# Kernel optimization log

Hardware: AMD Instinct MI355X
Metric: run time of the kernel (lower is better)

Reference implementation:

```python
import jax, jax.numpy as jnp
import numpy as np

NUM_GRAPHS = 64
NEG_SLOPE_EDGE = 0.2   # GATLayer alpha
NEG_SLOPE_READ = 0.01  # torch default leaky_relu slope in ReadoutLayer


def leaky_relu(x, slope):
    return jnp.where(x >= 0, x, slope * x)


def segment_softmax(e, seg, n):
    # numerically stable softmax of edge logits grouped by destination node
    m = jax.ops.segment_max(e, seg, num_segments=n)
    m = jnp.where(jnp.isfinite(m), m, 0.0)  # guard nodes with no in-edges
    ex = jnp.exp(e - m[seg])
    s = jax.ops.segment_sum(ex, seg, num_segments=n)
    return ex / jnp.where(s > 0, s, 1.0)[seg]


def gat_layer(h, src, dst, e_feat, W, a):
    n = h.shape[0]
    out = W.shape[1]
    z = h @ W                                      # [N, out]
    a_src, a_dst, a_e = a[:out], a[out:2 * out], a[2 * out:]
    # concat([z_src, z_dst, e_feat]) @ a  ==  z_src@a_src + z_dst@a_dst + e@a_e
    logits = leaky_relu(z[src] @ a_src + z[dst] @ a_dst + e_feat @ a_e,
                        NEG_SLOPE_EDGE)            # [E]
    alpha = segment_softmax(logits, dst, n)        # [E]
    msg = alpha[:, None] * z[src]                  # [E, out]
    return jax.ops.segment_sum(msg, dst, num_segments=n)  # [N, out]


def readout(h, gid, w_att, b_att):
    # DGL mean_nodes(g, 'z', 'att'): multiply feat by weight, then mean per graph
    att = jnp.exp(leaky_relu(h @ w_att + b_att, NEG_SLOPE_READ))  # [N]
    num = jax.ops.segment_sum(att[:, None] * h, gid, num_segments=NUM_GRAPHS)
    cnt = jax.ops.segment_sum(jnp.ones_like(att), gid, num_segments=NUM_GRAPHS)
    return num / jnp.maximum(cnt, 1.0)[:, None]    # [G, hidden]


def setup_inputs() -> dict:
    key = jax.random.key(0)
    ks = jax.random.split(key, 16)
    N, E, F_IN, H, ED, C = 50000, 800000, 128, 128, 16, 10
    sc = lambda f: np.float32(1.0 / np.sqrt(f))
    return {
        "x": jax.random.normal(ks[0], (N, F_IN), jnp.float32),
        "e_feat": jax.random.normal(ks[1], (E, ED), jnp.float32),
        "src": jax.random.randint(ks[2], (E,), 0, N, dtype=jnp.int32),
        "dst": jax.random.randint(ks[3], (E,), 0, N, dtype=jnp.int32),
        "gid": jnp.sort(jax.random.randint(ks[4], (N,), 0, NUM_GRAPHS, dtype=jnp.int32)),
        "W1": jax.random.normal(ks[5], (F_IN, H), jnp.float32) * sc(F_IN),
        "a1": jax.random.normal(ks[6], (2 * H + ED,), jnp.float32) * sc(2 * H + ED),
        "W2": jax.random.normal(ks[7], (H, H), jnp.float32) * sc(H),
        "a2": jax.random.normal(ks[8], (2 * H + ED,), jnp.float32) * sc(2 * H + ED),
        "W3": jax.random.normal(ks[9], (H, H), jnp.float32) * sc(H),
        "a3": jax.random.normal(ks[10], (2 * H + ED,), jnp.float32) * sc(2 * H + ED),
        "w_att": jax.random.normal(ks[11], (H,), jnp.float32) * sc(H),
        "b_att": jnp.zeros((), jnp.float32),
        "W_cls": jax.random.normal(ks[12], (3 * H, C), jnp.float32) * sc(3 * H),
        "b_cls": jnp.zeros((C,), jnp.float32),
    }


def reference(x, e_feat, src, dst, gid, W1, a1, W2, a2, W3, a3,
              w_att, b_att, W_cls, b_cls):
    # dropout is identity at inference (training=False)
    h1 = jax.nn.relu(gat_layer(x, src, dst, e_feat, W1, a1))
    hg1 = readout(h1, gid, w_att, b_att)
    h2 = jax.nn.relu(gat_layer(h1, src, dst, e_feat, W2, a2))
    hg2 = readout(h2, gid, w_att, b_att)
    h3 = jax.nn.relu(gat_layer(h2, src, dst, e_feat, W3, a3))
    hg3 = readout(h3, gid, w_att, b_att)
    y = jnp.concatenate([hg1, hg2, hg3], axis=1) @ W_cls + b_cls  # [G, C]
    return jax.nn.log_softmax(y, axis=1)
```

## Files before the change

### kernel.cpp

```cpp
#include <hip/hip_runtime.h>
#include <math.h>

#define HD 128
#define ED 16
#define NG 64
#define NC 10
#define HK 8

typedef short bf16x8 __attribute__((ext_vector_type(8)));
typedef float f32x4 __attribute__((ext_vector_type(4)));

__device__ __forceinline__ unsigned short f2b(float x){
  unsigned u = __float_as_uint(x);
  unsigned r = (u + 0x7fffu + ((u >> 16) & 1u)) >> 16;
  return (unsigned short)r;
}
__device__ __forceinline__ float blo(unsigned p){ return __uint_as_float(p << 16); }
__device__ __forceinline__ float bhi(unsigned p){ return __uint_as_float(p & 0xffff0000u); }
__device__ __forceinline__ float bperm_f(int idx, float v){
  return __int_as_float(__builtin_amdgcn_ds_bpermute(idx<<2, __float_as_int(v)));
}
__device__ __forceinline__ int bperm_i(int idx, int v){
  return __builtin_amdgcn_ds_bpermute(idx<<2, v);
}
__device__ __forceinline__ bf16x8 ld8f32_bf16(const float* p){
  float4 u0 = *(const float4*)p;
  float4 u1 = *(const float4*)(p+4);
  uint4 o;
  o.x = f2b(u0.x) | ((unsigned)f2b(u0.y)<<16);
  o.y = f2b(u0.z) | ((unsigned)f2b(u0.w)<<16);
  o.z = f2b(u1.x) | ((unsigned)f2b(u1.y)<<16);
  o.w = f2b(u1.z) | ((unsigned)f2b(u1.w)<<16);
  return __builtin_bit_cast(bf16x8, o);
}

__global__ __launch_bounds__(256) void k_pre(
    const int* __restrict__ dst, int* __restrict__ h, int Nr,
    int* __restrict__ rank, int E, int NH, int NE4,
    const int* __restrict__ src, const float* __restrict__ ef,
    const float* __restrict__ a1e, const float* __restrict__ a2e,
    const float* __restrict__ a3e, uint2* __restrict__ pay,
    const float* __restrict__ W1, const float* __restrict__ W2, const float* __restrict__ W3,
    unsigned short* __restrict__ Wb,
    const int* __restrict__ gid, float* __restrict__ cnt,
    float* __restrict__ hg,
    int N){
  int b = blockIdx.x;
  if(b < NH){
    int xcc;
    asm volatile("s_getreg_b32 %0, hwreg(HW_REG_XCC_ID, 0, 4)" : "=s"(xcc));
    xcc &= (HK-1);
    int* hk = h + (size_t)xcc*Nr;
    int tag = xcc << 24;
    int e4 = (b*256 + threadIdx.x)*4;
    if(e4+3 < E){
      int4 d = *(const int4*)&dst[e4];
      int4 r;
      r.x = __hip_atomic_fetch_add(&hk[d.x], 1, __ATOMIC_RELAXED, __HIP_MEMORY_SCOPE_WORKGROUP) | tag;
      r.y = __hip_atomic_fetch_add(&hk[d.y], 1, __ATOMIC_RELAXED, __HIP_MEMORY_SCOPE_WORKGROUP) | tag;
      r.z = __hip_atomic_fetch_add(&hk[d.z], 1, __ATOMIC_RELAXED, __HIP_MEMORY_SCOPE_WORKGROUP) | tag;
      r.w = __hip_atomic_fetch_add(&hk[d.w], 1, __ATOMIC_RELAXED, __HIP_MEMORY_SCOPE_WORKGROUP) | tag;
      *(int4*)&rank[e4] = r;
    } else {
      for(int k=0;k<4;k++) if(e4+k<E)
        rank[e4+k] = __hip_atomic_fetch_add(&hk[dst[e4+k]], 1, __ATOMIC_RELAXED, __HIP_MEMORY_SCOPE_WORKGROUP) | tag;
    }
    return;
  }
  b -= NH;
  if(b < NE4){
    int t = b*256 + threadIdx.x;
    int e = t >> 2;
    int sub = t & 3;
    if(e >= E) return;
    float4 f  = *(const float4*)&ef[(size_t)e*ED + sub*4];
    float4 A1 = *(const float4*)&a1e[sub*4];
    float4 A2 = *(const float4*)&a2e[sub*4];
    float4 A3 = *(const float4*)&a3e[sub*4];
    float q1 = fmaf(f.x,A1.x, fmaf(f.y,A1.y, fmaf(f.z,A1.z, f.w*A1.w)));
    float q2 = fmaf(f.x,A2.x, fmaf(f.y,A2.y, fmaf(f.z,A2.z, f.w*A2.w)));
    float q3 = fmaf(f.x,A3.x, fmaf(f.y,A3.y, fmaf(f.z,A3.z, f.w*A3.w)));
    q1 += __shfl_xor(q1,1); q1 += __shfl_xor(q1,2);
    q2 += __shfl_xor(q2,1); q2 += __shfl_xor(q2,2);
    q3 += __shfl_xor(q3,1); q3 += __shfl_xor(q3,2);
    if(sub == 0){
      uint2 A;
      A.x = (unsigned)f2b(q1) | ((unsigned)f2b(q2) << 16);
      A.y = (unsigned)src[e] | ((unsigned)f2b(q3) << 16);
      pay[e] = A;
    }
    return;
  }
  b -= NE4;
  if(b < 24){
    int idx = b*256 + threadIdx.x;
    if(idx >= 3*2048) return;
    int layer = idx >> 11;
    int r = idx & 2047;
    const float* W = (layer==0)?W1:((layer==1)?W2:W3);
    int lane = r & 63, tile = r >> 6;
    int kt = tile >> 3, nt = tile & 7;
    int qq = lane >> 4, cc = lane & 15;
    int kbase = kt*32 + qq*8;
    int col = nt*16 + cc;
    unsigned short tmp[8];
    #pragma unroll
    for(int j=0;j<8;j++) tmp[j] = f2b(W[(size_t)(kbase+j)*HD + col]);
    uint4 o;
    o.x = tmp[0]|((unsigned)tmp[1]<<16); o.y = tmp[2]|((unsigned)tmp[3]<<16);
    o.z = tmp[4]|((unsigned)tmp[5]<<16); o.w = tmp[6]|((unsigned)tmp[7]<<16);
    *(uint4*)&Wb[(size_t)idx*8] = o;
    return;
  }
  b -= 24;
  if(b == 0){
    int g = threadIdx.x;
    if(g >= NG) return;
    int lo=0, hi=N;
    while(lo<hi){ int mid=(lo+hi)>>1; if(gid[mid] < g) lo=mid+1; else hi=mid; }
    int start = lo; lo = start; hi = N;
    while(lo<hi){ int mid=(lo+hi)>>1; if(gid[mid] < g+1) lo=mid+1; else hi=mid; }
    cnt[g] = (float)(lo - start);
    return;
  }
  b -= 1;
  int i = (b*256 + threadIdx.x)*4;
  if(i < 3*NG*HD) *(float4*)&hg[i] = (float4){0.f,0.f,0.f,0.f};
}

__global__ __launch_bounds__(64) void k_bsum(const int* __restrict__ h, int Nr,
                                             int* __restrict__ deg,
                                             int* __restrict__ bsum, int N){
  int b = blockIdx.x, t = threadIdx.x;
  int i = b*256 + t*4;
  int d0=0,d1=0,d2=0,d3=0;
  if(i+3 < N){
    #pragma unroll
    for(int k=0;k<HK;k++){
      int4 v = *(const int4*)&h[(size_t)k*Nr + i];
      d0+=v.x; d1+=v.y; d2+=v.z; d3+=v.w;
    }
    int4 o; o.x=d0; o.y=d1; o.z=d2; o.w=d3;
    *(int4*)&deg[i] = o;
  } else {
    int tmp[4] = {0,0,0,0};
    for(int j=0;j<4;j++) if(i+j<N){
      int s2=0;
      for(int k=0;k<HK;k++) s2 += h[(size_t)k*Nr + i + j];
      deg[i+j]=s2; tmp[j]=s2;
    }
    d0=tmp[0]; d1=tmp[1]; d2=tmp[2]; d3=tmp[3];
  }
  int s = d0+d1+d2+d3;
  #pragma unroll
  for(int o=32;o;o>>=1) s += __shfl_xor(s,o);
  if(t==0) bsum[b] = s;
}

__global__ __launch_bounds__(256) void k_bprop2(const int* __restrict__ deg,
                                                const int* __restrict__ bsum,
                                                const int* __restrict__ h, int Nr,
                                                int* __restrict__ offs,
                                                int* __restrict__ offs2,
                                                int N, int E){
  __shared__ int sh[256];
  __shared__ int sbase;
  int b = blockIdx.x, t = threadIdx.x;
  int s = 0;
  for(int j=t; j<b; j+=256) s += bsum[j];
  #pragma unroll
  for(int o=32;o;o>>=1) s += __shfl_xor(s,o);
  if(t < 4) sh[t] = 0;
  __syncthreads();
  if((t&63)==0) sh[t>>6] = s;
  __syncthreads();
  if(t==0) sbase = sh[0]+sh[1]+sh[2]+sh[3];
  __syncthreads();
  int i = b*256 + t;
  int v = (i<N) ? deg[i] : 0;
  sh[t] = v; __syncthreads();
  for(int o=1;o<256;o<<=1){ int u = (t>=o)?sh[t-o]:0; __syncthreads(); sh[t]+=u; __syncthreads(); }
  if(i<N){
    int base = sbase + sh[t] - v;
    offs[i] = base;
    int run = base;
    #pragma unroll
    for(int k=0;k<HK;k++){
      offs2[(size_t)k*Nr + i] = run;
      run += h[(size_t)k*Nr + i];
    }
  }
  if(b==0 && t==0) offs[N] = E;
}


__device__ __forceinline__ void scatter_dev(int bidx,
                           const int* __restrict__ dst, const int* __restrict__ rank,
                           const uint2* __restrict__ pay,
                           const int* __restrict__ offs2, int Nr,
                           uint2* __restrict__ rec, int E){
  int e = bidx*256 + threadIdx.x;
  if(e >= E) return;
  int d = dst[e];
  unsigned rk = (unsigned)rank[e];
  int k = (int)(rk >> 24);
  int p = offs2[(size_t)k*Nr + d] + (int)(rk & 0xffffffu);
  rec[p] = pay[e];
}

__device__ __forceinline__ void gemm_dev(int bidx,
    const unsigned short* __restrict__ Ab,
    const float* __restrict__ Af,
    const unsigned short* __restrict__ Wb,
    unsigned short* __restrict__ Zb,
    const float* __restrict__ avec,
    float* __restrict__ ps, float* __restrict__ pd, int M)
{
  int tid = threadIdx.x;
  int w = tid >> 6, lane = tid & 63;
  int q = lane >> 4, c = lane & 15;
  int rowbase = bidx*128 + w*32;
  f32x4 acc[2][8];
  #pragma unroll
  for(int t=0;t<2;t++)
    #pragma unroll
    for(int n=0;n<8;n++) acc[t][n] = (f32x4){0.f,0.f,0.f,0.f};

  int r0 = rowbase + c;      if(r0 > M-1) r0 = M-1;
  int r1 = rowbase + 16 + c; if(r1 > M-1) r1 = M-1;
  #pragma unroll
  for(int kt=0; kt<4; kt++){
    int ko = kt*32 + q*8;
    bf16x8 a0, a1;
    if(Af){
      a0 = ld8f32_bf16(&Af[(size_t)r0*HD + ko]);
      a1 = ld8f32_bf16(&Af[(size_t)r1*HD + ko]);
    } else {
      a0 = __builtin_bit_cast(bf16x8, *(const uint4*)&Ab[(size_t)r0*HD + ko]);
      a1 = __builtin_bit_cast(bf16x8, *(const uint4*)&Ab[(size_t)r1*HD + ko]);
    }
    #pragma unroll
    for(int n=0;n<8;n++){
      bf16x8 b = __builtin_bit_cast(bf16x8, *(const uint4*)&Wb[(((size_t)(kt*8+n))*64 + lane)*8]);
      acc[0][n] = __builtin_amdgcn_mfma_f32_16x16x32_bf16(a0, b, acc[0][n], 0,0,0);
      acc[1][n] = __builtin_amdgcn_mfma_f32_16x16x32_bf16(a1, b, acc[1][n], 0,0,0);
    }
  }
  float asv[8], adv[8];
  #pragma unroll
  for(int n=0;n<8;n++){ asv[n] = avec[n*16+c]; adv[n] = avec[HD + n*16+c]; }
  #pragma unroll
  for(int t=0;t<2;t++){
    #pragma unroll
    for(int r=0;r<4;r++){
      int grow = rowbase + t*16 + 4*q + r;
      bool ok = grow < M;
      #pragma unroll
      for(int n=0;n<8;n++){
        if(ok) Zb[(size_t)grow*HD + n*16 + c] = f2b(acc[t][n][r]);
      }
      float pp = 0.f, dd = 0.f;
      #pragma unroll
      for(int n=0;n<8;n++){ pp = fmaf(acc[t][n][r], asv[n], pp); dd = fmaf(acc[t][n][r], adv[n], dd); }
      #pragma unroll
      for(int o=1;o<16;o<<=1){ pp += __shfl_xor(pp,o); dd += __shfl_xor(dd,o); }
      if(ok && c==0){ ps[grow] = pp; pd[grow] = dd; }
    }
  }
}

#define RCH 16
__device__ __forceinline__ void readout_dev(int rb,
                          const unsigned* __restrict__ hbu,
                          const float* __restrict__ att,
                          const int* __restrict__ gid,
                          float* __restrict__ hg, int N){
  int g = rb >> 2;
  int chunk = ((rb & 3) << 2) + (threadIdx.x >> 6);
  int t = threadIdx.x & 63;
  int lo=0, hi=N;
  while(lo<hi){ int mid=(lo+hi)>>1; if(gid[mid] < g) lo=mid+1; else hi=mid; }
  int start = lo; lo = start; hi = N;
  while(lo<hi){ int mid=(lo+hi)>>1; if(gid[mid] < g+1) lo=mid+1; else hi=mid; }
  int end = lo;
  int len = end - start;
  int c0 = start + (int)(((long long)len * chunk) / RCH);
  int c1 = start + (int)(((long long)len * (chunk+1)) / RCH);
  float acc0 = 0.f, acc1 = 0.f;
  for(int v=c0; v<c1; v++){
    unsigned P = hbu[(size_t)v*64 + t];
    float a = att[v];
    acc0 = fmaf(a, blo(P), acc0);
    acc1 = fmaf(a, bhi(P), acc1);
  }
  atomicAdd(&hg[g*HD + 2*t],     acc0);
  atomicAdd(&hg[g*HD + 2*t + 1], acc1);
}

__global__ __launch_bounds__(256) void k_sg1(
    const float* __restrict__ x, const unsigned short* __restrict__ Wb,
    unsigned short* __restrict__ Zb, const float* __restrict__ avec,
    float* __restrict__ ps, float* __restrict__ pd, int M, int GB,
    const int* __restrict__ dst, const int* __restrict__ rank,
    const uint2* __restrict__ pay,
    const int* __restrict__ offs2, int Nr, uint2* __restrict__ rec, int E){
  if(blockIdx.x < GB) gemm_dev(blockIdx.x, (const unsigned short*)0, x, Wb, Zb, avec, ps, pd, M);
  else scatter_dev(blockIdx.x - GB, dst, rank, pay, offs2, Nr, rec, E);
}

__global__ __launch_bounds__(256) void k_rg(
    const unsigned short* __restrict__ Ab, const unsigned short* __restrict__ Wb,
    unsigned short* __restrict__ Zb, const float* __restrict__ avec,
    float* __restrict__ ps, float* __restrict__ pd, int M, int GB,
    const unsigned* __restrict__ hbu, const float* __restrict__ att,
    const int* __restrict__ gid, float* __restrict__ hg, int N){
  if(blockIdx.x < GB) gemm_dev(blockIdx.x, Ab, (const float*)0, Wb, Zb, avec, ps, pd, M);
  else readout_dev(blockIdx.x - GB, hbu, att, gid, hg, N);
}

__global__ __launch_bounds__(256) void k_agg2(const uint4* __restrict__ zb4,
                                              const int* __restrict__ offs,
                                              const uint2* __restrict__ rec,
                                              const float* __restrict__ ps,
                                              const float* __restrict__ pd,
                                              int layer,
                                              unsigned* __restrict__ hbu,
                                              float* __restrict__ att,
                                              const float* __restrict__ watt,
                                              const float* __restrict__ batt, int N){
  int wid = blockIdx.x*4 + (threadIdx.x>>6);
  int lane = threadIdx.x & 63;
  if(wid >= N) return;
  int q = lane >> 4, c = lane & 15;
  int d0 = offs[wid], d1 = offs[wid+1];
  float pdv = pd[wid];
  float acc[8];
  #pragma unroll
  for(int i=0;i<8;i++) acc[i]=0.f;
  float ssum = 0.f;

  for(int t0=d0; t0<d1; t0+=64){
    int rem = d1 - t0; if(rem > 64) rem = 64;
    int j = t0 + lane;
    float w = 0.f; int u = 0;
    if(j < d1){
      uint2 R = rec[j];
      u = (int)(R.y & 0xffffu);
      unsigned qb = (layer==0) ? (R.x & 0xffffu) : (layer==1 ? (R.x >> 16) : (R.y >> 16));
      float ql = __uint_as_float(qb << 16);
      float l = ps[u] + pdv + ql;
      l = (l >= 0.f) ? l : 0.2f*l;
      w = __expf(l);
    }
    float ws = w;
    #pragma unroll
    for(int o=32;o;o>>=1) ws += __shfl_xor(ws,o);
    ssum += ws;
    for(int jb=0; jb<rem; jb+=16){
      float w0 = bperm_f(jb+q,    w);  int u0 = bperm_i(jb+q,    u);
      float w1 = bperm_f(jb+4+q,  w);  int u1 = bperm_i(jb+4+q,  u);
      float w2 = bperm_f(jb+8+q,  w);  int u2 = bperm_i(jb+8+q,  u);
      float w3 = bperm_f(jb+12+q, w);  int u3 = bperm_i(jb+12+q, u);
      uint4 P0 = zb4[(size_t)u0*16 + c];
      uint4 P1 = zb4[(size_t)u1*16 + c];
      uint4 P2 = zb4[(size_t)u2*16 + c];
      uint4 P3 = zb4[(size_t)u3*16 + c];
      acc[0] = fmaf(w0, blo(P0.x), acc[0]); acc[1] = fmaf(w0, bhi(P0.x), acc[1]);
      acc[2] = fmaf(w0, blo(P0.y), acc[2]); acc[3] = fmaf(w0, bhi(P0.y), acc[3]);
      acc[4] = fmaf(w0, blo(P0.z), acc[4]); acc[5] = fmaf(w0, bhi(P0.z), acc[5]);
      acc[6] = fmaf(w0, blo(P0.w), acc[6]); acc[7] = fmaf(w0, bhi(P0.w), acc[7]);
      acc[0] = fmaf(w1, blo(P1.x), acc[0]); acc[1] = fmaf(w1, bhi(P1.x), acc[1]);
      acc[2] = fmaf(w1, blo(P1.y), acc[2]); acc[3] = fmaf(w1, bhi(P1.y), acc[3]);
      acc[4] = fmaf(w1, blo(P1.z), acc[4]); acc[5] = fmaf(w1, bhi(P1.z), acc[5]);
      acc[6] = fmaf(w1, blo(P1.w), acc[6]); acc[7] = fmaf(w1, bhi(P1.w), acc[7]);
      acc[0] = fmaf(w2, blo(P2.x), acc[0]); acc[1] = fmaf(w2, bhi(P2.x), acc[1]);
      acc[2] = fmaf(w2, blo(P2.y), acc[2]); acc[3] = fmaf(w2, bhi(P2.y), acc[3]);
      acc[4] = fmaf(w2, blo(P2.z), acc[4]); acc[5] = fmaf(w2, bhi(P2.z), acc[5]);
      acc[6] = fmaf(w2, blo(P2.w), acc[6]); acc[7] = fmaf(w2, bhi(P2.w), acc[7]);
      acc[0] = fmaf(w3, blo(P3.x), acc[0]); acc[1] = fmaf(w3, bhi(P3.x), acc[1]);
      acc[2] = fmaf(w3, blo(P3.y), acc[2]); acc[3] = fmaf(w3, bhi(P3.y), acc[3]);
      acc[4] = fmaf(w3, blo(P3.z), acc[4]); acc[5] = fmaf(w3, bhi(P3.z), acc[5]);
      acc[6] = fmaf(w3, blo(P3.w), acc[6]); acc[7] = fmaf(w3, bhi(P3.w), acc[7]);
    }
  }
  #pragma unroll
  for(int i=0;i<8;i++){ acc[i] += __shfl_xor(acc[i],16); acc[i] += __shfl_xor(acc[i],32); }
  float inv = (d1 > d0) ? 1.0f/ssum : 0.0f;
  #pragma unroll
  for(int i=0;i<8;i++) acc[i] = fmaxf(acc[i]*inv, 0.f);
  hbu[(size_t)wid*64 + c*4 + q] = (unsigned)f2b(acc[2*q]) | ((unsigned)f2b(acc[2*q+1])<<16);
  float4 w0v = *(const float4*)&watt[c*8];
  float4 w1v = *(const float4*)&watt[c*8+4];
  float t = acc[0]*w0v.x + acc[1]*w0v.y + acc[2]*w0v.z + acc[3]*w0v.w
          + acc[4]*w1v.x + acc[5]*w1v.y + acc[6]*w1v.z + acc[7]*w1v.w;
  #pragma unroll
  for(int o=1;o<16;o<<=1) t += __shfl_xor(t,o);
  t += batt[0];
  float lr = (t >= 0.f) ? t : 0.01f*t;
  if(lane==0) att[wid] = __expf(lr);
}

__global__ __launch_bounds__(64) void k_readout(const unsigned* __restrict__ hbu,
                                                const float* __restrict__ att,
                                                const int* __restrict__ gid,
                                                float* __restrict__ hg, int N){
  int g = blockIdx.x / RCH;
  int chunk = blockIdx.x % RCH;
  int t = threadIdx.x;
  int lo=0, hi=N;
  while(lo<hi){ int mid=(lo+hi)>>1; if(gid[mid] < g) lo=mid+1; else hi=mid; }
  int start = lo; lo = start; hi = N;
  while(lo<hi){ int mid=(lo+hi)>>1; if(gid[mid] < g+1) lo=mid+1; else hi=mid; }
  int end = lo;
  int len = end - start;
  int c0 = start + (int)(((long long)len * chunk) / RCH);
  int c1 = start + (int)(((long long)len * (chunk+1)) / RCH);
  float acc0 = 0.f, acc1 = 0.f;
  for(int v=c0; v<c1; v++){
    unsigned P = hbu[(size_t)v*64 + t];
    float a = att[v];
    acc0 = fmaf(a, blo(P), acc0);
    acc1 = fmaf(a, bhi(P), acc1);
  }
  atomicAdd(&hg[g*HD + 2*t],     acc0);
  atomicAdd(&hg[g*HD + 2*t + 1], acc1);
}

__global__ __launch_bounds__(384) void k_final(const float* __restrict__ hg,
                                               const float* __restrict__ cnt,
                                               const float* __restrict__ Wc,
                                               const float* __restrict__ bc,
                                               float* __restrict__ out){
  int g = blockIdx.x;
  int t = threadIdx.x;
  __shared__ float red[6];
  __shared__ float yv[NC];
  float invc = 1.f / fmaxf(cnt[g], 1.f);
  int part = t >> 7;
  int f = t & 127;
  float v = hg[(size_t)part*NG*HD + g*HD + f] * invc;
  for(int c=0; c<NC; c++){
    float p = v * Wc[(size_t)t*NC + c];
    #pragma unroll
    for(int o=32;o;o>>=1) p += __shfl_xor(p,o);
    if((t&63)==0) red[t>>6] = p;
    __syncthreads();
    if(t==0) yv[c] = bc[c] + red[0]+red[1]+red[2]+red[3]+red[4]+red[5];
    __syncthreads();
  }
  if(t==0){
    float mx = -INFINITY;
    #pragma unroll
    for(int c=0;c<NC;c++) mx = fmaxf(mx, yv[c]);
    float s = 0.f;
    #pragma unroll
    for(int c=0;c<NC;c++) s += __expf(yv[c] - mx);
    float ls = logf(s);
    #pragma unroll
    for(int c=0;c<NC;c++) out[g*NC + c] = yv[c] - mx - ls;
  }
}

extern "C" void kernel_launch(void* const* d_in, const int* in_sizes, int n_in,
                              void* d_out, int out_size, void* d_ws, size_t ws_size,
                              hipStream_t stream) {
  const float* x     = (const float*)d_in[0];
  const float* efeat = (const float*)d_in[1];
  const int*   src   = (const int*)d_in[2];
  const int*   dst   = (const int*)d_in[3];
  const int*   gid   = (const int*)d_in[4];
  const float* W1    = (const float*)d_in[5];
  const float* a1    = (const float*)d_in[6];
  const float* W2    = (const float*)d_in[7];
  const float* a2    = (const float*)d_in[8];
  const float* W3    = (const float*)d_in[9];
  const float* a3    = (const float*)d_in[10];
  const float* watt  = (const float*)d_in[11];
  const float* batt  = (const float*)d_in[12];
  const float* Wc    = (const float*)d_in[13];
  const float* bc    = (const float*)d_in[14];
  float* out = (float*)d_out;

  int N = in_sizes[4];
  int E = in_sizes[2];
  int Nr = (N + 63) & ~63;

  char* p = (char*)d_ws;
  auto alloc = [&](size_t bytes)->void*{
    void* r = (void*)p;
    p += (bytes + 255) & ~(size_t)255;
    return r;
  };
  unsigned short* Hb = (unsigned short*)alloc((size_t)N*HD*2);
  unsigned short* Zb = (unsigned short*)alloc((size_t)N*HD*2);
  unsigned short* Wball = (unsigned short*)alloc((size_t)3*2048*8*2);
  float* ps      = (float*)alloc((size_t)N*4);
  float* pd      = (float*)alloc((size_t)N*4);
  float* att     = (float*)alloc((size_t)N*4);
  int*   deg     = (int*)  alloc((size_t)N*4);
  int*   offs    = (int*)  alloc((size_t)(N+1)*4);
  int*   offs2   = (int*)  alloc((size_t)Nr*HK*4);
  int*   h       = (int*)  alloc((size_t)Nr*HK*4);
  int*   rank    = (int*)  alloc((size_t)E*4);
  uint2* pay     = (uint2*)alloc((size_t)E*8);
  uint2* rec     = (uint2*)alloc((size_t)E*8);
  int*   bsum    = (int*)  alloc((size_t)1024*4);
  float* hg      = (float*)alloc((size_t)3*NG*HD*4);
  float* cnt     = (float*)alloc((size_t)NG*4);
  (void)ws_size; (void)n_in; (void)out_size;

  int nwblocks = (N + 3) / 4;
  int nb = (N + 255) / 256;
  int NH = (E/4 + 255) / 256;
  int NE4 = (E*4 + 255) / 256;
  int GB = (N + 127) / 128;
  int SB = (E + 255) / 256;

  hipMemsetAsync(h, 0, (size_t)Nr*HK*4, stream);
  k_pre<<<NH + NE4 + 24 + 1 + 24, 256, 0, stream>>>(dst, h, Nr, rank, E, NH, NE4,
                                                    src, efeat, a1+2*HD, a2+2*HD, a3+2*HD, pay,
                                                    W1, W2, W3, Wball,
                                                    gid, cnt, hg, N);
  k_bsum<<<nb, 64, 0, stream>>>(h, Nr, deg, bsum, N);
  k_bprop2<<<nb, 256, 0, stream>>>(deg, bsum, h, Nr, offs, offs2, N, E);
  k_sg1<<<GB + SB, 256, 0, stream>>>(x, Wball, Zb, a1, ps, pd, N, GB,
                                     dst, rank, pay, offs2, Nr, rec, E);
  k_agg2<<<nwblocks, 256, 0, stream>>>((const uint4*)Zb, offs, rec, ps, pd, 0,
                                       (unsigned*)Hb, att, watt, batt, N);
  k_rg<<<GB + NG*4, 256, 0, stream>>>(Hb, Wball + (size_t)1*2048*8, Zb, a2, ps, pd, N, GB,
                                      (const unsigned*)Hb, att, gid, hg + 0*NG*HD, N);
  k_agg2<<<nwblocks, 256, 0, stream>>>((const uint4*)Zb, offs, rec, ps, pd, 1,
                                       (unsigned*)Hb, att, watt, batt, N);
  k_rg<<<GB + NG*4, 256, 0, stream>>>(Hb, Wball + (size_t)2*2048*8, Zb, a3, ps, pd, N, GB,
                                      (const unsigned*)Hb, att, gid, hg + 1*NG*HD, N);
  k_agg2<<<nwblocks, 256, 0, stream>>>((const uint4*)Zb, offs, rec, ps, pd, 2,
                                       (unsigned*)Hb, att, watt, batt, N);
  k_readout<<<NG*RCH, 64, 0, stream>>>((const unsigned*)Hb, att, gid,
                                       hg + 2*NG*HD, N);
  k_final<<<NG, 384, 0, stream>>>(hg, cnt, Wc, bc, out);
}
```

Measured before the change: 398.2 us.

## Replace global per-XCC atomic histogram with LDS-chunked per-block histograms

The in-degree count for the CSR build no longer uses global atomics into eight per-XCC histograms. Each block now takes a contiguous chunk of 16K edges and histograms it in shared memory with packed 16-bit counters, making several passes over the node range. It writes per-block 16-bit counts, and the rank is derived from the edge's block index. The degree-sum step is folded into k_pre, which drops the memset and the k_bsum launch. In exchange, each block rereads its dst chunk once per node pass, and the prefix and scatter steps loop over about 49 block histograms instead of 8.

New measurement: 448.6 us. 12.7% more time.

```diff
diff --git a/kernel.cpp b/kernel.cpp
--- a/kernel.cpp
+++ b/kernel.cpp
@@ -5,7 +5,8 @@
 #define ED 16
 #define NG 64
 #define NC 10
-#define HK 8
+#define EPB_LOG 14
+#define EPB (1<<EPB_LOG)
 
 typedef short bf16x8 __attribute__((ext_vector_type(8)));
 typedef float f32x4 __attribute__((ext_vector_type(4)));
@@ -34,9 +35,38 @@
   return __builtin_bit_cast(bf16x8, o);
 }
 
+__global__ __launch_bounds__(256) void k_hist(const int* __restrict__ dst,
+                                              unsigned short* __restrict__ H16, int Nr2,
+                                              int* __restrict__ rank, int E, int N){
+  __shared__ unsigned hls[EPB/2];
+  int kb = blockIdx.x;
+  int e0 = kb << EPB_LOG;
+  int e1 = e0 + EPB; if(e1 > E) e1 = E;
+  int npass = (N + EPB - 1) >> EPB_LOG;
+  for(int ps=0; ps<npass; ps++){
+    int h0 = ps << EPB_LOG;
+    for(int w=threadIdx.x; w<EPB/2; w+=256) hls[w] = 0u;
+    __syncthreads();
+    for(int e=e0+threadIdx.x; e<e1; e+=256){
+      int d = dst[e];
+      unsigned rel = (unsigned)(d - h0);
+      if(rel < (unsigned)EPB){
+        unsigned add = (rel & 1u) ? 0x10000u : 1u;
+        unsigned old = atomicAdd(&hls[rel>>1], add);
+        rank[e] = (int)((old >> ((rel & 1u)*16u)) & 0xffffu);
+      }
+    }
+    __syncthreads();
+    int nodes = N - h0; if(nodes > EPB) nodes = EPB;
+    int words = (nodes + 1) >> 1;
+    unsigned* Hg = (unsigned*)(H16 + (size_t)kb*Nr2 + h0);
+    for(int w=threadIdx.x; w<words; w+=256) Hg[w] = hls[w];
+    __syncthreads();
+  }
+}
+
 __global__ __launch_bounds__(256) void k_pre(
-    const int* __restrict__ dst, int* __restrict__ h, int Nr,
-    int* __restrict__ rank, int E, int NH, int NE4,
+    int NE4, int E,
     const int* __restrict__ src, const float* __restrict__ ef,
     const float* __restrict__ a1e, const float* __restrict__ a2e,
     const float* __restrict__ a3e, uint2* __restrict__ pay,
@@ -44,30 +74,10 @@
     unsigned short* __restrict__ Wb,
     const int* __restrict__ gid, float* __restrict__ cnt,
     float* __restrict__ hg,
+    const unsigned short* __restrict__ H16, int Nr2, int NB,
+    int* __restrict__ deg, int* __restrict__ bsum,
     int N){
   int b = blockIdx.x;
-  if(b < NH){
-    int xcc;
-    asm volatile("s_getreg_b32 %0, hwreg(HW_REG_XCC_ID, 0, 4)" : "=s"(xcc));
-    xcc &= (HK-1);
-    int* hk = h + (size_t)xcc*Nr;
-    int tag = xcc << 24;
-    int e4 = (b*256 + threadIdx.x)*4;
-    if(e4+3 < E){
-      int4 d = *(const int4*)&dst[e4];
-      int4 r;
-      r.x = __hip_atomic_fetch_add(&hk[d.x], 1, __ATOMIC_RELAXED, __HIP_MEMORY_SCOPE_WORKGROUP) | tag;
-      r.y = __hip_atomic_fetch_add(&hk[d.y], 1, __ATOMIC_RELAXED, __HIP_MEMORY_SCOPE_WORKGROUP) | tag;
-      r.z = __hip_atomic_fetch_add(&hk[d.z], 1, __ATOMIC_RELAXED, __HIP_MEMORY_SCOPE_WORKGROUP) | tag;
-      r.w = __hip_atomic_fetch_add(&hk[d.w], 1, __ATOMIC_RELAXED, __HIP_MEMORY_SCOPE_WORKGROUP) | tag;
-      *(int4*)&rank[e4] = r;
-    } else {
-      for(int k=0;k<4;k++) if(e4+k<E)
-        rank[e4+k] = __hip_atomic_fetch_add(&hk[dst[e4+k]], 1, __ATOMIC_RELAXED, __HIP_MEMORY_SCOPE_WORKGROUP) | tag;
-    }
-    return;
-  }
-  b -= NH;
   if(b < NE4){
     int t = b*256 + threadIdx.x;
     int e = t >> 2;
@@ -124,45 +134,34 @@
     return;
   }
   b -= 1;
-  int i = (b*256 + threadIdx.x)*4;
-  if(i < 3*NG*HD) *(float4*)&hg[i] = (float4){0.f,0.f,0.f,0.f};
-}
-
-__global__ __launch_bounds__(64) void k_bsum(const int* __restrict__ h, int Nr,
-                                             int* __restrict__ deg,
-                                             int* __restrict__ bsum, int N){
-  int b = blockIdx.x, t = threadIdx.x;
-  int i = b*256 + t*4;
-  int d0=0,d1=0,d2=0,d3=0;
-  if(i+3 < N){
-    #pragma unroll
-    for(int k=0;k<HK;k++){
-      int4 v = *(const int4*)&h[(size_t)k*Nr + i];
-      d0+=v.x; d1+=v.y; d2+=v.z; d3+=v.w;
-    }
-    int4 o; o.x=d0; o.y=d1; o.z=d2; o.w=d3;
-    *(int4*)&deg[i] = o;
-  } else {
-    int tmp[4] = {0,0,0,0};
-    for(int j=0;j<4;j++) if(i+j<N){
-      int s2=0;
-      for(int k=0;k<HK;k++) s2 += h[(size_t)k*Nr + i + j];
-      deg[i+j]=s2; tmp[j]=s2;
-    }
-    d0=tmp[0]; d1=tmp[1]; d2=tmp[2]; d3=tmp[3];
-  }
-  int s = d0+d1+d2+d3;
-  #pragma unroll
-  for(int o=32;o;o>>=1) s += __shfl_xor(s,o);
-  if(t==0) bsum[b] = s;
+  if(b < 24){
+    int i = (b*256 + threadIdx.x)*4;
+    if(i < 3*NG*HD) *(float4*)&hg[i] = (float4){0.f,0.f,0.f,0.f};
+    return;
+  }
+  b -= 24;
+  {
+    __shared__ int rs[4];
+    int i = b*256 + threadIdx.x;
+    int s = 0;
+    if(i < N){
+      for(int k=0;k<NB;k++) s += (int)H16[(size_t)k*Nr2 + i];
+      deg[i] = s;
+    }
+    #pragma unroll
+    for(int o=32;o;o>>=1) s += __shfl_xor(s,o);
+    if((threadIdx.x&63)==0) rs[threadIdx.x>>6] = s;
+    __syncthreads();
+    if(threadIdx.x==0) bsum[b] = rs[0]+rs[1]+rs[2]+rs[3];
+  }
 }
 
 __global__ __launch_bounds__(256) void k_bprop2(const int* __restrict__ deg,
                                                 const int* __restrict__ bsum,
-                                                const int* __restrict__ h, int Nr,
+                                                const unsigned short* __restrict__ H16, int Nr2,
                                                 int* __restrict__ offs,
-                                                int* __restrict__ offs2,
-                                                int N, int E){
+                                                int* __restrict__ offs2, int Nr,
+                                                int N, int E, int NB){
   __shared__ int sh[256];
   __shared__ int sbase;
   int b = blockIdx.x, t = threadIdx.x;
@@ -184,10 +183,9 @@
     int base = sbase + sh[t] - v;
     offs[i] = base;
     int run = base;
-    #pragma unroll
-    for(int k=0;k<HK;k++){
+    for(int k=0;k<NB;k++){
       offs2[(size_t)k*Nr + i] = run;
-      run += h[(size_t)k*Nr + i];
+      run += (int)H16[(size_t)k*Nr2 + i];
     }
   }
   if(b==0 && t==0) offs[N] = E;
@@ -202,9 +200,8 @@
   int e = bidx*256 + threadIdx.x;
   if(e >= E) return;
   int d = dst[e];
-  unsigned rk = (unsigned)rank[e];
-  int k = (int)(rk >> 24);
-  int p = offs2[(size_t)k*Nr + d] + (int)(rk & 0xffffffu);
+  int k = e >> EPB_LOG;
+  int p = offs2[(size_t)k*Nr + d] + rank[e];
   rec[p] = pay[e];
 }
 
@@ -484,6 +481,9 @@
   int N = in_sizes[4];
   int E = in_sizes[2];
   int Nr = (N + 63) & ~63;
+  int NB = (E + EPB - 1) >> EPB_LOG;
+  int NP = (N + EPB - 1) >> EPB_LOG;
+  int Nr2 = NP << EPB_LOG;
 
   char* p = (char*)d_ws;
   auto alloc = [&](size_t bytes)->void*{
@@ -499,8 +499,8 @@
   float* att     = (float*)alloc((size_t)N*4);
   int*   deg     = (int*)  alloc((size_t)N*4);
   int*   offs    = (int*)  alloc((size_t)(N+1)*4);
-  int*   offs2   = (int*)  alloc((size_t)Nr*HK*4);
-  int*   h       = (int*)  alloc((size_t)Nr*HK*4);
+  int*   offs2   = (int*)  alloc((size_t)NB*Nr*4);
+  unsigned short* H16 = (unsigned short*)alloc((size_t)NB*Nr2*2);
   int*   rank    = (int*)  alloc((size_t)E*4);
   uint2* pay     = (uint2*)alloc((size_t)E*8);
   uint2* rec     = (uint2*)alloc((size_t)E*8);
@@ -511,18 +511,17 @@
 
   int nwblocks = (N + 3) / 4;
   int nb = (N + 255) / 256;
-  int NH = (E/4 + 255) / 256;
   int NE4 = (E*4 + 255) / 256;
   int GB = (N + 127) / 128;
   int SB = (E + 255) / 256;
 
-  hipMemsetAsync(h, 0, (size_t)Nr*HK*4, stream);
-  k_pre<<<NH + NE4 + 24 + 1 + 24, 256, 0, stream>>>(dst, h, Nr, rank, E, NH, NE4,
+  k_hist<<<NB, 256, 0, stream>>>(dst, H16, Nr2, rank, E, N);
+  k_pre<<<NE4 + 24 + 1 + 24 + nb, 256, 0, stream>>>(NE4, E,
                                                     src, efeat, a1+2*HD, a2+2*HD, a3+2*HD, pay,
                                                     W1, W2, W3, Wball,
-                                                    gid, cnt, hg, N);
-  k_bsum<<<nb, 64, 0, stream>>>(h, Nr, deg, bsum, N);
-  k_bprop2<<<nb, 256, 0, stream>>>(deg, bsum, h, Nr, offs, offs2, N, E);
+                                                    gid, cnt, hg,
+                                                    H16, Nr2, NB, deg, bsum, N);
+  k_bprop2<<<nb, 256, 0, stream>>>(deg, bsum, H16, Nr2, offs, offs2, Nr, N, E, NB);
   k_sg1<<<GB + SB, 256, 0, stream>>>(x, Wball, Zb, a1, ps, pd, N, GB,
                                      dst, rank, pay, offs2, Nr, rec, E);
   k_agg2<<<nwblocks, 256, 0, stream>>>((const uint4*)Zb, offs, rec, ps, pd, 0,
```
